# Kernel optimization log

Hardware: AMD Instinct MI355X
Metric: run time of the kernel (lower is better)

Reference implementation:

```python
import jax, jax.numpy as jnp
import numpy as np

N_HEADS = 16
N_KV_HEADS = 4
N_EMBED = 2048
HEAD_DIM = 128
SECTIONS = [16, 24, 24, 16, 24, 24]


def _process_rotary(c):
    # c: [3, B, T, HEAD_DIM] -> [B, 1, T, HEAD_DIM]
    splits = np.cumsum(SECTIONS)[:-1]
    secs = jnp.split(c, splits, axis=-1)
    out = jnp.concatenate([s[i % 3] for i, s in enumerate(secs)], axis=-1)
    return out[:, None]  # add head axis


def _rotate_half(x):
    x1, x2 = jnp.split(x, 2, axis=-1)
    return jnp.concatenate([-x2, x1], axis=-1)


def setup_inputs() -> dict:
    key = jax.random.key(0)
    ks = jax.random.split(key, 12)
    B, T = 1, 2048
    s = 0.02
    return {
        "x": jax.random.normal(ks[0], (B, T, N_EMBED), jnp.float32),
        "cos": jax.random.uniform(ks[1], (3, B, T, HEAD_DIM), jnp.float32),
        "sin": jax.random.uniform(ks[2], (3, B, T, HEAD_DIM), jnp.float32),
        "Wq": jax.random.normal(ks[3], (N_EMBED, N_EMBED), jnp.float32) * s,
        "bq": jax.random.normal(ks[4], (N_EMBED,), jnp.float32) * s,
        "Wk": jax.random.normal(ks[5], (N_EMBED, N_KV_HEADS * HEAD_DIM), jnp.float32) * s,
        "bk": jax.random.normal(ks[6], (N_KV_HEADS * HEAD_DIM,), jnp.float32) * s,
        "Wv": jax.random.normal(ks[7], (N_EMBED, N_KV_HEADS * HEAD_DIM), jnp.float32) * s,
        "bv": jax.random.normal(ks[8], (N_KV_HEADS * HEAD_DIM,), jnp.float32) * s,
        "Wo": jax.random.normal(ks[9], (N_EMBED, N_EMBED), jnp.float32) * s,
    }


def reference(x, cos, sin, Wq, bq, Wk, bk, Wv, bv, Wo):
    B, T, C = x.shape
    H, Hkv, D = N_HEADS, N_KV_HEADS, HEAD_DIM
    q = (x @ Wq + bq).reshape(B, T, H, D).transpose(0, 2, 1, 3)    # [B,H,T,D]
    k = (x @ Wk + bk).reshape(B, T, Hkv, D).transpose(0, 2, 1, 3)  # [B,Hkv,T,D]
    v = (x @ Wv + bv).reshape(B, T, Hkv, D).transpose(0, 2, 1, 3)
    # multi-section rope (cos/sin are 4-dim -> custom path)
    c = _process_rotary(cos)
    s = _process_rotary(sin)
    q = q * c + _rotate_half(q) * s
    k = k * c + _rotate_half(k) * s
    present_k, present_v = k, v
    # GQA expansion (repeat_interleave over head axis)
    r = H // Hkv
    k = jnp.repeat(k, r, axis=1)
    v = jnp.repeat(v, r, axis=1)
    # causal SDPA
    scores = jnp.einsum("bhqd,bhkd->bhqk", q, k) / jnp.sqrt(jnp.float32(D))
    causal = jnp.tril(jnp.ones((T, T), dtype=bool))
    scores = jnp.where(causal, scores, jnp.finfo(scores.dtype).min)
    attn = jax.nn.softmax(scores, axis=-1)
    y = jnp.einsum("bhqk,bhkd->bhqd", attn, v)
    y = y.transpose(0, 2, 1, 3).reshape(B, T, C)
    y = y @ Wo
    return (y, present_k, present_v)
```

## Files before the change

kernel.cpp:

```cpp
#include <hip/hip_runtime.h>

typedef unsigned short u16;
typedef unsigned int u32;
typedef __attribute__((ext_vector_type(4))) float f32x4;
typedef __attribute__((ext_vector_type(8))) __bf16 bf16x8;
typedef __attribute__((ext_vector_type(4))) u16 u16x4;
typedef __attribute__((ext_vector_type(2))) u32 u32x2;


__device__ __forceinline__ u16 f2bf(float f) {
  union { float f; unsigned u; } v; v.f = f;
  unsigned r = v.u + 0x7fffu + ((v.u >> 16) & 1u);
  return (u16)(r >> 16);
}

__device__ __forceinline__ u32 pack_bf2(float a, float b) {
  union { float f; unsigned u; } x, y;
  x.f = a; y.f = b;
#if __has_builtin(__builtin_amdgcn_perm)
  return __builtin_amdgcn_perm(y.u + 0x8000u, x.u + 0x8000u, 0x07060302u);
#else
  return (u32)((x.u + 0x8000u) >> 16) | ((y.u + 0x8000u) & 0xffff0000u);
#endif
}

__device__ __forceinline__ void stage16(const void* g, void* l) {
#if __has_builtin(__builtin_amdgcn_global_load_lds)
  __builtin_amdgcn_global_load_lds((const __attribute__((address_space(1))) void*)g,
                                   (__attribute__((address_space(3))) void*)l, 16, 0, 0);
#else
  *(f32x4*)l = *(const f32x4*)g;
#endif
}

__device__ __forceinline__ f32x4 mfma16(bf16x8 a, bf16x8 b, f32x4 c) {
  return __builtin_amdgcn_mfma_f32_16x16x32_bf16(a, b, c, 0, 0, 0);
}

__device__ __forceinline__ float fexp2(float x) {
#if __has_builtin(__builtin_amdgcn_exp2f)
  return __builtin_amdgcn_exp2f(x);
#else
  return exp2f(x);
#endif
}

__device__ __forceinline__ int rope_ch(int d) {
  int dd = (d < 64) ? d : d - 64;
  return (dd < 16) ? 0 : (dd < 40 ? 1 : 2);
}


__global__ void yuna_convert_prep(const float* __restrict__ in, u16* __restrict__ out,
                                  const float* __restrict__ cosp, const float* __restrict__ sinp,
                                  float* __restrict__ csel, float* __restrict__ ssel) {
  int b = blockIdx.x;
  if (b < 4096) {
    int i = b * 256 + threadIdx.x;
    f32x4 v = ((const f32x4*)in)[i];
    u16x4 o;
    o.x = f2bf(v.x); o.y = f2bf(v.y); o.z = f2bf(v.z); o.w = f2bf(v.w);
    ((u16x4*)out)[i] = o;
  } else {
    int i = (b - 4096) * 256 + threadIdx.x;
    int i4 = i * 4;
    int t = i4 >> 7, d = i4 & 127;
    f32x4 c, s;
#pragma unroll
    for (int j = 0; j < 4; ++j) {
      int ch = rope_ch(d + j);
      c[j] = cosp[(size_t)ch * 262144 + (size_t)t * 128 + d + j];
      s[j] = sinp[(size_t)ch * 262144 + (size_t)t * 128 + d + j];
    }
    ((f32x4*)csel)[i] = c;
    ((f32x4*)ssel)[i] = s;
  }
}

__global__ void yuna_prep_weights(const float* __restrict__ Wq, const float* __restrict__ Wk,
                                  const float* __restrict__ Wv, const float* __restrict__ Wo,
                                  u16* __restrict__ Wb, u16* __restrict__ Wob) {
  __shared__ float tile[64][65];
  const int mat = blockIdx.z;
  const float* W;
  u16* out;
  int N;
  if (mat == 0)      { W = Wq; out = Wb;                          N = 2048; }
  else if (mat == 1) { W = Wk; out = Wb + (size_t)2048 * 2048;    N = 512; }
  else if (mat == 2) { W = Wv; out = Wb + (size_t)2560 * 2048;    N = 512; }
  else               { W = Wo; out = Wob;                         N = 2048; }
  int k0 = blockIdx.x * 64, n0 = blockIdx.y * 64;
  if (n0 >= N) return;
  int tx = threadIdx.x & 63, ty = threadIdx.x >> 6;
#pragma unroll
  for (int j = 0; j < 64; j += 4)
    tile[ty + j][tx] = W[(size_t)(k0 + ty + j) * N + n0 + tx];
  __syncthreads();
#pragma unroll
  for (int j = 0; j < 64; j += 4)
    out[(size_t)(n0 + ty + j) * 2048 + k0 + tx] = f2bf(tile[tx][ty + j]);
}

__global__ __launch_bounds__(256, 3) void yuna_gemm_qkv(
    const u16* __restrict__ A, const u16* __restrict__ Bt,
    const float* __restrict__ bq, const float* __restrict__ bk, const float* __restrict__ bv,
    const float* __restrict__ csel, const float* __restrict__ ssel,
    u16* __restrict__ qb, u16* __restrict__ kb, u16* __restrict__ vtb,
    float* __restrict__ pk, float* __restrict__ pv) {
  const int K = 2048;
  __shared__ __align__(16) char smem[49152];
  const int tid = threadIdx.x;
  const int wave = tid >> 6, lane = tid & 63;
  const int lrow = lane & 15, lkg = lane >> 4;
  const int m0 = blockIdx.x * 64;
  const int by = blockIdx.y;
  const int n0 = by * 128;
  const int sw = lrow & 7;

  const int srow = tid >> 3;
  const int ssc = (tid & 7) ^ ((tid >> 3) & 7);
  const size_t abase = (size_t)(m0 + srow) * K + ssc * 8;
  const size_t bbase = (size_t)(n0 + srow) * K + ssc * 8;

  const f32x4 fzero = {0.f, 0.f, 0.f, 0.f};
  f32x4 acc[4][2];
#pragma unroll
  for (int mi = 0; mi < 4; ++mi) { acc[mi][0] = fzero; acc[mi][1] = fzero; }

#pragma unroll
  for (int it = 0; it < 2; ++it)
    stage16(A + abase + (size_t)it * 32 * K, smem + (tid + it * 256) * 16);
#pragma unroll
  for (int it = 0; it < 4; ++it)
    stage16(Bt + bbase + (size_t)it * 32 * K, smem + 16384 + (tid + it * 256) * 16);

  for (int k0 = 0, ki = 0; k0 < K; k0 += 64, ++ki) {
    const int cur = ki & 1;
    const char* Asb = smem + cur * 8192;
    const char* Bsb = smem + 16384 + cur * 16384;
    if (k0 + 64 < K) {
      char* Asn = smem + (cur ^ 1) * 8192;
      char* Bsn = smem + 16384 + (cur ^ 1) * 16384;
#pragma unroll
      for (int it = 0; it < 2; ++it)
        stage16(A + abase + (size_t)it * 32 * K + k0 + 64, Asn + (tid + it * 256) * 16);
#pragma unroll
      for (int it = 0; it < 4; ++it)
        stage16(Bt + bbase + (size_t)it * 32 * K + k0 + 64, Bsn + (tid + it * 256) * 16);
      asm volatile("s_waitcnt vmcnt(6)\n\ts_barrier" ::: "memory");
    } else {
      asm volatile("s_waitcnt vmcnt(0)\n\ts_barrier" ::: "memory");
    }
#pragma unroll
    for (int kk = 0; kk < 2; ++kk) {
      const int cof = ((kk * 4 + lkg) ^ sw) << 4;
      bf16x8 af[4], bfr[2];
#pragma unroll
      for (int mi = 0; mi < 4; ++mi)
        af[mi] = *(const bf16x8*)(Asb + (mi * 16 + lrow) * 128 + cof);
#pragma unroll
      for (int ni = 0; ni < 2; ++ni)
        bfr[ni] = *(const bf16x8*)(Bsb + (wave * 16 + ni * 64 + lrow) * 128 + cof);
#pragma unroll
      for (int mi = 0; mi < 4; ++mi)
#pragma unroll
        for (int ni = 0; ni < 2; ++ni)
          acc[mi][ni] = mfma16(af[mi], bfr[ni], acc[mi][ni]);
    }
    asm volatile("s_barrier" ::: "memory");
  }

  if (by >= 20) {
    const int kvh = by - 20;
#pragma unroll
    for (int mi = 0; mi < 4; ++mi)
#pragma unroll
      for (int ni = 0; ni < 2; ++ni) {
        int d = wave * 16 + ni * 64 + lrow;
        float bb = bv[kvh * 128 + d];
        int mb = mi * 16 + lkg * 4;
        float v0 = acc[mi][ni][0] + bb, v1 = acc[mi][ni][1] + bb;
        float v2 = acc[mi][ni][2] + bb, v3 = acc[mi][ni][3] + bb;
        size_t pb = ((size_t)(kvh * 2048 + m0 + mb)) * 128 + d;
        pv[pb] = v0; pv[pb + 128] = v1; pv[pb + 256] = v2; pv[pb + 384] = v3;
        u16x4 w;
        w.x = f2bf(v0); w.y = f2bf(v1); w.z = f2bf(v2); w.w = f2bf(v3);
        *(u16x4*)(vtb + ((size_t)(kvh * 128 + d)) * 2048 + m0 + mb) = w;
      }
  } else {
    const float QSCALE = 1.4426950408889634f * 0.08838834764831845f;
    const bool isQ = (by < 16);
    const int h = isQ ? by : (by - 16);
    const float* bias = isQ ? bq : bk;
    const int dlo = wave * 16 + lrow;
    const float blo = bias[h * 128 + dlo];
    const float bhi = bias[h * 128 + dlo + 64];
#pragma unroll
    for (int mi = 0; mi < 4; ++mi) {
      const int tb = m0 + mi * 16 + lkg * 4;
#pragma unroll
      for (int r = 0; r < 4; ++r) {
        const int t = tb + r;
        float a = acc[mi][0][r] + blo;
        float b = acc[mi][1][r] + bhi;
        size_t cb = (size_t)t * 128 + dlo;
        float cl = csel[cb], sl = ssel[cb];
        float ch = csel[cb + 64], sh = ssel[cb + 64];
        float lo = a * cl - b * sl;
        float hi = b * ch + a * sh;
        size_t o = (((size_t)(h * 2048 + t)) << 7) + dlo;
        if (isQ) {
          qb[o] = f2bf(lo * QSCALE);
          qb[o + 64] = f2bf(hi * QSCALE);
        } else {
          kb[o] = f2bf(lo);
          kb[o + 64] = f2bf(hi);
          pk[o] = lo; pk[o + 64] = hi;
        }
      }
    }
  }
}

__global__ __launch_bounds__(256, 3) void yuna_gemm_out(
    const u16* __restrict__ A, const u16* __restrict__ Bt, float* __restrict__ C) {
  const int K = 2048;
  __shared__ __align__(16) char smem[49152];
  const int tid = threadIdx.x;
  const int wave = tid >> 6, lane = tid & 63;
  const int lrow = lane & 15, lkg = lane >> 4;
  const int m0 = blockIdx.x * 64;
  const int n0 = blockIdx.y * 128;
  const int wc = wave * 32;
  const int sw = lrow & 7;

  const int srow = tid >> 3;
  const int ssc = (tid & 7) ^ ((tid >> 3) & 7);
  const size_t abase = (size_t)(m0 + srow) * K + ssc * 8;
  const size_t bbase = (size_t)(n0 + srow) * K + ssc * 8;

  const f32x4 fzero = {0.f, 0.f, 0.f, 0.f};
  f32x4 acc[4][2];
#pragma unroll
  for (int mi = 0; mi < 4; ++mi) { acc[mi][0] = fzero; acc[mi][1] = fzero; }

#pragma unroll
  for (int it = 0; it < 2; ++it)
    stage16(A + abase + (size_t)it * 32 * K, smem + (tid + it * 256) * 16);
#pragma unroll
  for (int it = 0; it < 4; ++it)
    stage16(Bt + bbase + (size_t)it * 32 * K, smem + 16384 + (tid + it * 256) * 16);

  for (int k0 = 0, ki = 0; k0 < K; k0 += 64, ++ki) {
    const int cur = ki & 1;
    const char* Asb = smem + cur * 8192;
    const char* Bsb = smem + 16384 + cur * 16384;
    if (k0 + 64 < K) {
      char* Asn = smem + (cur ^ 1) * 8192;
      char* Bsn = smem + 16384 + (cur ^ 1) * 16384;
#pragma unroll
      for (int it = 0; it < 2; ++it)
        stage16(A + abase + (size_t)it * 32 * K + k0 + 64, Asn + (tid + it * 256) * 16);
#pragma unroll
      for (int it = 0; it < 4; ++it)
        stage16(Bt + bbase + (size_t)it * 32 * K + k0 + 64, Bsn + (tid + it * 256) * 16);
      asm volatile("s_waitcnt vmcnt(6)\n\ts_barrier" ::: "memory");
    } else {
      asm volatile("s_waitcnt vmcnt(0)\n\ts_barrier" ::: "memory");
    }
#pragma unroll
    for (int kk = 0; kk < 2; ++kk) {
      const int cof = ((kk * 4 + lkg) ^ sw) << 4;
      bf16x8 af[4], bfr[2];
#pragma unroll
      for (int mi = 0; mi < 4; ++mi)
        af[mi] = *(const bf16x8*)(Asb + (mi * 16 + lrow) * 128 + cof);
#pragma unroll
      for (int ni = 0; ni < 2; ++ni)
        bfr[ni] = *(const bf16x8*)(Bsb + (wc + ni * 16 + lrow) * 128 + cof);
#pragma unroll
      for (int mi = 0; mi < 4; ++mi)
#pragma unroll
        for (int ni = 0; ni < 2; ++ni)
          acc[mi][ni] = mfma16(af[mi], bfr[ni], acc[mi][ni]);
    }
    asm volatile("s_barrier" ::: "memory");
  }
#pragma unroll
  for (int mi = 0; mi < 4; ++mi)
#pragma unroll
    for (int ni = 0; ni < 2; ++ni) {
      int d = wc + ni * 16 + lrow;
      int mb = mi * 16 + lkg * 4;
#pragma unroll
      for (int r = 0; r < 4; ++r)
        C[(size_t)(m0 + mb + r) * 2048 + n0 + d] = acc[mi][ni][r];
    }
}

__global__ __launch_bounds__(256, 2) void yuna_flash_attn(
    const u16* __restrict__ Q,
    const u16* __restrict__ Kb,
    const u16* __restrict__ Vt,
    u16* __restrict__ Y) {
  __shared__ __align__(16) u16 Ks[2][64 * 128];
  __shared__ __align__(16) u16 Vs[2][128 * 64];
  __shared__ __align__(16) u16 Ps[64 * 64];
  const int h = blockIdx.x;
  const int yb = blockIdx.y;
  const int qb = (yb < 16) ? yb : 47 - yb;
  const int kvh = h >> 2;
  const int tid = threadIdx.x, wave = tid >> 6, lane = tid & 63;
  const int lrow = lane & 15, lkg = lane >> 4;
  const int m = wave * 16 + lrow;
  const int sw = lrow & 7;

  const int krow = tid >> 4;
  const int ksc = (tid & 15) ^ ((tid >> 4) & 7);
  const size_t kbase0 = ((size_t)(kvh * 2048 + krow) << 7) + ksc * 8;
  const int vrow = tid >> 3;
  const int vsc = (tid & 7) ^ ((tid >> 3) & 7);
  const size_t vbase0 = (size_t)(kvh * 128 + vrow) * 2048 + vsc * 8;

  bf16x8 qf[4];
#pragma unroll
  for (int kk = 0; kk < 4; ++kk)
    qf[kk] = *(const bf16x8*)(Q + (((size_t)h * 2048 + qb * 64 + m) << 7) + kk * 32 + lkg * 8);

  const f32x4 fzero = {0.f, 0.f, 0.f, 0.f};
  f32x4 o[8];
#pragma unroll
  for (int dt = 0; dt < 8; ++dt) o[dt] = fzero;
  float m_i = -1e30f, l_i = 0.f;

  const int nkb = qb + 1;

#pragma unroll
  for (int it = 0; it < 4; ++it)
    stage16(Kb + kbase0 + ((size_t)(it * 16) << 7), (char*)Ks[0] + (tid + it * 256) * 16);
#pragma unroll
  for (int it = 0; it < 4; ++it)
    stage16(Vt + vbase0 + (size_t)it * 32 * 2048, (char*)Vs[0] + (tid + it * 256) * 16);

  for (int kb = 0; kb < nkb; ++kb) {
    const int cur = kb & 1;
    const char* Ksb = (const char*)Ks[cur];
    const char* Vsb = (const char*)Vs[cur];
    if (kb + 1 < nkb) {
      char* Ksn = (char*)Ks[cur ^ 1];
      char* Vsn = (char*)Vs[cur ^ 1];
#pragma unroll
      for (int it = 0; it < 4; ++it)
        stage16(Kb + kbase0 + ((size_t)((kb + 1) * 64 + it * 16) << 7), Ksn + (tid + it * 256) * 16);
#pragma unroll
      for (int it = 0; it < 4; ++it)
        stage16(Vt + vbase0 + (size_t)it * 32 * 2048 + (kb + 1) * 64, Vsn + (tid + it * 256) * 16);
      asm volatile("s_waitcnt vmcnt(8)\n\ts_barrier" ::: "memory");
    } else {
      asm volatile("s_waitcnt vmcnt(0)\n\ts_barrier" ::: "memory");
    }

    f32x4 s[4];
#pragma unroll
    for (int nt = 0; nt < 4; ++nt) s[nt] = fzero;
#pragma unroll
    for (int kk = 0; kk < 4; ++kk) {
      const int cof = ((kk * 4 + lkg) ^ sw) << 4;
      bf16x8 kf[4];
#pragma unroll
      for (int nt = 0; nt < 4; ++nt)
        kf[nt] = *(const bf16x8*)(Ksb + (nt * 16 + lrow) * 256 + cof);
#pragma unroll
      for (int nt = 0; nt < 4; ++nt)
        s[nt] = mfma16(kf[nt], qf[kk], s[nt]);
    }
    if (kb == qb) {
#pragma unroll
      for (int nt = 0; nt < 4; ++nt)
#pragma unroll
        for (int r = 0; r < 4; ++r)
          if (nt * 16 + lkg * 4 + r > m) s[nt][r] = -1e30f;
    }

    float mx = -1e30f;
#pragma unroll
    for (int nt = 0; nt < 4; ++nt)
#pragma unroll
      for (int r = 0; r < 4; ++r) mx = fmaxf(mx, s[nt][r]);
    mx = fmaxf(mx, __shfl_xor(mx, 16));
    mx = fmaxf(mx, __shfl_xor(mx, 32));
    float mnew = fmaxf(m_i, mx);
    float alpha = fexp2(m_i - mnew);
    m_i = mnew;
    float ps = 0.f;
    const int hh = lkg & 1;
#pragma unroll
    for (int nt = 0; nt < 4; ++nt) {
      float p0 = fexp2(s[nt][0] - mnew);
      float p1 = fexp2(s[nt][1] - mnew);
      float p2 = fexp2(s[nt][2] - mnew);
      float p3 = fexp2(s[nt][3] - mnew);
      ps += (p0 + p1) + (p2 + p3);
      u32x2 pk2;
      pk2.x = pack_bf2(p0, p1);
      pk2.y = pack_bf2(p2, p3);
      int cc = 2 * nt + (lkg >> 1);
      *(u32x2*)((char*)Ps + m * 128 + ((cc ^ (m & 7)) << 4) + hh * 8) = pk2;
    }
    ps += __shfl_xor(ps, 16);
    ps += __shfl_xor(ps, 32);
    l_i = l_i * alpha + ps;
#pragma unroll
    for (int dt = 0; dt < 8; ++dt) o[dt] *= alpha;

#pragma unroll
    for (int kk = 0; kk < 2; ++kk) {
      const int cof = ((kk * 4 + lkg) ^ sw) << 4;
      bf16x8 pf = *(const bf16x8*)((char*)Ps + m * 128 + cof);
      bf16x8 vf[8];
#pragma unroll
      for (int dt = 0; dt < 8; ++dt)
        vf[dt] = *(const bf16x8*)(Vsb + (dt * 16 + lrow) * 128 + cof);
#pragma unroll
      for (int dt = 0; dt < 8; ++dt)
        o[dt] = mfma16(vf[dt], pf, o[dt]);
    }
    asm volatile("s_barrier" ::: "memory");
  }

  __syncthreads();
  {
    float inv = 1.f / l_i;
    const int hh = lkg & 1;
#pragma unroll
    for (int dt = 0; dt < 8; ++dt) {
      u32x2 w2;
      w2.x = pack_bf2(o[dt][0] * inv, o[dt][1] * inv);
      w2.y = pack_bf2(o[dt][2] * inv, o[dt][3] * inv);
      int cc = 2 * dt + (lkg >> 1);
      *(u32x2*)((char*)Ks[0] + m * 256 + ((cc ^ (m & 7)) << 4) + hh * 8) = w2;
    }
  }
  __syncthreads();
#pragma unroll
  for (int it = 0; it < 4; ++it) {
    int c = tid + it * 256;
    int row = c >> 4, cc = c & 15;
    f32x4 v = *(const f32x4*)((const char*)Ks[0] + row * 256 + ((cc ^ (row & 7)) << 4));
    *(f32x4*)(Y + (size_t)(qb * 64 + row) * 2048 + h * 128 + cc * 8) = v;
  }
}


extern "C" void kernel_launch(void* const* d_in, const int* in_sizes, int n_in,
                              void* d_out, int out_size, void* d_ws, size_t ws_size,
                              hipStream_t stream) {
  const float* x = (const float*)d_in[0];
  const float* cosp = (const float*)d_in[1];
  const float* sinp = (const float*)d_in[2];
  const float* Wq = (const float*)d_in[3];
  const float* bq = (const float*)d_in[4];
  const float* Wk = (const float*)d_in[5];
  const float* bk = (const float*)d_in[6];
  const float* Wv = (const float*)d_in[7];
  const float* bv = (const float*)d_in[8];
  const float* Wo = (const float*)d_in[9];
  float* out = (float*)d_out;
  float* out_k = out + 4194304;
  float* out_v = out + 5242880;

  char* ws = (char*)d_ws;
  u16* xb   = (u16*)(ws + 0);
  u16* Wb   = (u16*)(ws + 8388608);
  u16* Wob  = (u16*)(ws + 20971520);
  float* csel = (float*)(ws + 29360128);
  float* ssel = (float*)(ws + 30408704);
  u16* qbuf = (u16*)(ws + 54525952);
  u16* kbuf = (u16*)(ws + 62914560);
  u16* vtb  = (u16*)(ws + 65011712);
  u16* yat  = (u16*)(ws + 67108864);

  yuna_convert_prep<<<4352, 256, 0, stream>>>(x, xb, cosp, sinp, csel, ssel);
  yuna_prep_weights<<<dim3(32, 32, 4), 256, 0, stream>>>(Wq, Wk, Wv, Wo, Wb, Wob);
  yuna_gemm_qkv<<<dim3(32, 24), 256, 0, stream>>>(xb, Wb, bq, bk, bv, csel, ssel,
                                                  qbuf, kbuf, vtb, out_k, out_v);
  yuna_flash_attn<<<dim3(16, 32), 256, 0, stream>>>(qbuf, kbuf, vtb, yat);
  yuna_gemm_out<<<dim3(32, 16), 256, 0, stream>>>(yat, Wob, out);
}
```

Measured before the change: 227.0 us.

## Replace direct-to-LDS double buffering with register-staged single-buffer prefetch in GEMMs

Both projection GEMM kernels stop issuing async global-to-LDS copies into a double-buffered 48KB shared area. They now prefetch the next K tile into registers while computing on a single 24KB LDS buffer, then write the registers to LDS between barriers. This halves the LDS footprint, which may allow more resident blocks, at the cost of extra VGPRs, an extra barrier per iteration, and less overlap between loads and LDS writes.

```diff
diff --git a/kernel.cpp b/kernel.cpp
--- a/kernel.cpp
+++ b/kernel.cpp
@@ -108,7 +108,8 @@
     u16* __restrict__ qb, u16* __restrict__ kb, u16* __restrict__ vtb,
     float* __restrict__ pk, float* __restrict__ pv) {
   const int K = 2048;
-  __shared__ __align__(16) char smem[49152];
+  __shared__ __align__(16) char As[8192];
+  __shared__ __align__(16) char Bs[16384];
   const int tid = threadIdx.x;
   const int wave = tid >> 6, lane = tid & 63;
   const int lrow = lane & 15, lkg = lane >> 4;
@@ -127,29 +128,30 @@
 #pragma unroll
   for (int mi = 0; mi < 4; ++mi) { acc[mi][0] = fzero; acc[mi][1] = fzero; }
 
+  f32x4 areg[2], breg[4];
 #pragma unroll
   for (int it = 0; it < 2; ++it)
-    stage16(A + abase + (size_t)it * 32 * K, smem + (tid + it * 256) * 16);
+    areg[it] = *(const f32x4*)(A + abase + (size_t)it * 32 * K);
 #pragma unroll
   for (int it = 0; it < 4; ++it)
-    stage16(Bt + bbase + (size_t)it * 32 * K, smem + 16384 + (tid + it * 256) * 16);
-
-  for (int k0 = 0, ki = 0; k0 < K; k0 += 64, ++ki) {
-    const int cur = ki & 1;
-    const char* Asb = smem + cur * 8192;
-    const char* Bsb = smem + 16384 + cur * 16384;
-    if (k0 + 64 < K) {
-      char* Asn = smem + (cur ^ 1) * 8192;
-      char* Bsn = smem + 16384 + (cur ^ 1) * 16384;
+    breg[it] = *(const f32x4*)(Bt + bbase + (size_t)it * 32 * K);
+#pragma unroll
+  for (int it = 0; it < 2; ++it)
+    *(f32x4*)(As + (tid + it * 256) * 16) = areg[it];
+#pragma unroll
+  for (int it = 0; it < 4; ++it)
+    *(f32x4*)(Bs + (tid + it * 256) * 16) = breg[it];
+  __syncthreads();
+
+  for (int k0 = 0; k0 < K; k0 += 64) {
+    const bool more = (k0 + 64 < K);
+    if (more) {
 #pragma unroll
       for (int it = 0; it < 2; ++it)
-        stage16(A + abase + (size_t)it * 32 * K + k0 + 64, Asn + (tid + it * 256) * 16);
+        areg[it] = *(const f32x4*)(A + abase + (size_t)it * 32 * K + k0 + 64);
 #pragma unroll
       for (int it = 0; it < 4; ++it)
-        stage16(Bt + bbase + (size_t)it * 32 * K + k0 + 64, Bsn + (tid + it * 256) * 16);
-      asm volatile("s_waitcnt vmcnt(6)\n\ts_barrier" ::: "memory");
-    } else {
-      asm volatile("s_waitcnt vmcnt(0)\n\ts_barrier" ::: "memory");
+        breg[it] = *(const f32x4*)(Bt + bbase + (size_t)it * 32 * K + k0 + 64);
     }
 #pragma unroll
     for (int kk = 0; kk < 2; ++kk) {
@@ -157,17 +159,26 @@
       bf16x8 af[4], bfr[2];
 #pragma unroll
       for (int mi = 0; mi < 4; ++mi)
-        af[mi] = *(const bf16x8*)(Asb + (mi * 16 + lrow) * 128 + cof);
+        af[mi] = *(const bf16x8*)(As + (mi * 16 + lrow) * 128 + cof);
 #pragma unroll
       for (int ni = 0; ni < 2; ++ni)
-        bfr[ni] = *(const bf16x8*)(Bsb + (wave * 16 + ni * 64 + lrow) * 128 + cof);
+        bfr[ni] = *(const bf16x8*)(Bs + (wave * 16 + ni * 64 + lrow) * 128 + cof);
 #pragma unroll
       for (int mi = 0; mi < 4; ++mi)
 #pragma unroll
         for (int ni = 0; ni < 2; ++ni)
           acc[mi][ni] = mfma16(af[mi], bfr[ni], acc[mi][ni]);
     }
-    asm volatile("s_barrier" ::: "memory");
+    __syncthreads();
+    if (more) {
+#pragma unroll
+      for (int it = 0; it < 2; ++it)
+        *(f32x4*)(As + (tid + it * 256) * 16) = areg[it];
+#pragma unroll
+      for (int it = 0; it < 4; ++it)
+        *(f32x4*)(Bs + (tid + it * 256) * 16) = breg[it];
+      __syncthreads();
+    }
   }
 
   if (by >= 20) {
@@ -225,7 +236,8 @@
 __global__ __launch_bounds__(256, 3) void yuna_gemm_out(
     const u16* __restrict__ A, const u16* __restrict__ Bt, float* __restrict__ C) {
   const int K = 2048;
-  __shared__ __align__(16) char smem[49152];
+  __shared__ __align__(16) char As[8192];
+  __shared__ __align__(16) char Bs[16384];
   const int tid = threadIdx.x;
   const int wave = tid >> 6, lane = tid & 63;
   const int lrow = lane & 15, lkg = lane >> 4;
@@ -244,29 +256,30 @@
 #pragma unroll
   for (int mi = 0; mi < 4; ++mi) { acc[mi][0] = fzero; acc[mi][1] = fzero; }
 
+  f32x4 areg[2], breg[4];
 #pragma unroll
   for (int it = 0; it < 2; ++it)
-    stage16(A + abase + (size_t)it * 32 * K, smem + (tid + it * 256) * 16);
+    areg[it] = *(const f32x4*)(A + abase + (size_t)it * 32 * K);
 #pragma unroll
   for (int it = 0; it < 4; ++it)
-    stage16(Bt + bbase + (size_t)it * 32 * K, smem + 16384 + (tid + it * 256) * 16);
-
-  for (int k0 = 0, ki = 0; k0 < K; k0 += 64, ++ki) {
-    const int cur = ki & 1;
-    const char* Asb = smem + cur * 8192;
-    const char* Bsb = smem + 16384 + cur * 16384;
-    if (k0 + 64 < K) {
-      char* Asn = smem + (cur ^ 1) * 8192;
-      char* Bsn = smem + 16384 + (cur ^ 1) * 16384;
+    breg[it] = *(const f32x4*)(Bt + bbase + (size_t)it * 32 * K);
+#pragma unroll
+  for (int it = 0; it < 2; ++it)
+    *(f32x4*)(As + (tid + it * 256) * 16) = areg[it];
+#pragma unroll
+  for (int it = 0; it < 4; ++it)
+    *(f32x4*)(Bs + (tid + it * 256) * 16) = breg[it];
+  __syncthreads();
+
+  for (int k0 = 0; k0 < K; k0 += 64) {
+    const bool more = (k0 + 64 < K);
+    if (more) {
 #pragma unroll
       for (int it = 0; it < 2; ++it)
-        stage16(A + abase + (size_t)it * 32 * K + k0 + 64, Asn + (tid + it * 256) * 16);
+        areg[it] = *(const f32x4*)(A + abase + (size_t)it * 32 * K + k0 + 64);
 #pragma unroll
       for (int it = 0; it < 4; ++it)
-        stage16(Bt + bbase + (size_t)it * 32 * K + k0 + 64, Bsn + (tid + it * 256) * 16);
-      asm volatile("s_waitcnt vmcnt(6)\n\ts_barrier" ::: "memory");
-    } else {
-      asm volatile("s_waitcnt vmcnt(0)\n\ts_barrier" ::: "memory");
+        breg[it] = *(const f32x4*)(Bt + bbase + (size_t)it * 32 * K + k0 + 64);
     }
 #pragma unroll
     for (int kk = 0; kk < 2; ++kk) {
@@ -274,17 +287,26 @@
       bf16x8 af[4], bfr[2];
 #pragma unroll
       for (int mi = 0; mi < 4; ++mi)
-        af[mi] = *(const bf16x8*)(Asb + (mi * 16 + lrow) * 128 + cof);
+        af[mi] = *(const bf16x8*)(As + (mi * 16 + lrow) * 128 + cof);
 #pragma unroll
       for (int ni = 0; ni < 2; ++ni)
-        bfr[ni] = *(const bf16x8*)(Bsb + (wc + ni * 16 + lrow) * 128 + cof);
+        bfr[ni] = *(const bf16x8*)(Bs + (wc + ni * 16 + lrow) * 128 + cof);
 #pragma unroll
       for (int mi = 0; mi < 4; ++mi)
 #pragma unroll
         for (int ni = 0; ni < 2; ++ni)
           acc[mi][ni] = mfma16(af[mi], bfr[ni], acc[mi][ni]);
     }
-    asm volatile("s_barrier" ::: "memory");
+    __syncthreads();
+    if (more) {
+#pragma unroll
+      for (int it = 0; it < 2; ++it)
+        *(f32x4*)(As + (tid + it * 256) * 16) = areg[it];
+#pragma unroll
+      for (int it = 0; it < 4; ++it)
+        *(f32x4*)(Bs + (tid + it * 256) * 16) = breg[it];
+      __syncthreads();
+    }
   }
 #pragma unroll
   for (int mi = 0; mi < 4; ++mi)
```

New measurement: 235.9 us. 1.04x slower.

## Widen QKV and output GEMM tiles to 64x256 per block

Applied to the files above, without the earlier changes.

Both GEMM kernels now compute a 64x256 output tile per block instead of 64x128, doubling the B-tile in shared memory and giving each wave a 4x4 MFMA accumulator grid. The aim is more reuse of the A tile per load and fewer blocks. The QKV epilogue is remapped so each wave pair handles one head, and the RoPE pairing and bias indexing change to match. In exchange, shared memory and register use rise, occupancy drops to 2 blocks per CU, and the grids shrink to 384 and 256 blocks, which may underfill the 256 CUs.

```diff
diff --git a/kernel.cpp b/kernel.cpp
--- a/kernel.cpp
+++ b/kernel.cpp
@@ -101,20 +101,20 @@
     out[(size_t)(n0 + ty + j) * 2048 + k0 + tx] = f2bf(tile[tx][ty + j]);
 }
 
-__global__ __launch_bounds__(256, 3) void yuna_gemm_qkv(
+__global__ __launch_bounds__(256, 2) void yuna_gemm_qkv(
     const u16* __restrict__ A, const u16* __restrict__ Bt,
     const float* __restrict__ bq, const float* __restrict__ bk, const float* __restrict__ bv,
     const float* __restrict__ csel, const float* __restrict__ ssel,
     u16* __restrict__ qb, u16* __restrict__ kb, u16* __restrict__ vtb,
     float* __restrict__ pk, float* __restrict__ pv) {
   const int K = 2048;
-  __shared__ __align__(16) char smem[49152];
+  __shared__ __align__(16) char smem[81920];
   const int tid = threadIdx.x;
   const int wave = tid >> 6, lane = tid & 63;
   const int lrow = lane & 15, lkg = lane >> 4;
   const int m0 = blockIdx.x * 64;
   const int by = blockIdx.y;
-  const int n0 = by * 128;
+  const int n0 = by * 256;
   const int sw = lrow & 7;
 
   const int srow = tid >> 3;
@@ -122,61 +122,67 @@
   const size_t abase = (size_t)(m0 + srow) * K + ssc * 8;
   const size_t bbase = (size_t)(n0 + srow) * K + ssc * 8;
 
+  const int rbase = (wave >> 1) * 128 + (wave & 1) * 32 + lrow;
+
   const f32x4 fzero = {0.f, 0.f, 0.f, 0.f};
-  f32x4 acc[4][2];
-#pragma unroll
-  for (int mi = 0; mi < 4; ++mi) { acc[mi][0] = fzero; acc[mi][1] = fzero; }
+  f32x4 acc[4][4];
+#pragma unroll
+  for (int mi = 0; mi < 4; ++mi)
+#pragma unroll
+    for (int ni = 0; ni < 4; ++ni) acc[mi][ni] = fzero;
 
 #pragma unroll
   for (int it = 0; it < 2; ++it)
     stage16(A + abase + (size_t)it * 32 * K, smem + (tid + it * 256) * 16);
 #pragma unroll
-  for (int it = 0; it < 4; ++it)
+  for (int it = 0; it < 8; ++it)
     stage16(Bt + bbase + (size_t)it * 32 * K, smem + 16384 + (tid + it * 256) * 16);
 
   for (int k0 = 0, ki = 0; k0 < K; k0 += 64, ++ki) {
     const int cur = ki & 1;
     const char* Asb = smem + cur * 8192;
-    const char* Bsb = smem + 16384 + cur * 16384;
+    const char* Bsb = smem + 16384 + cur * 32768;
     if (k0 + 64 < K) {
       char* Asn = smem + (cur ^ 1) * 8192;
-      char* Bsn = smem + 16384 + (cur ^ 1) * 16384;
+      char* Bsn = smem + 16384 + (cur ^ 1) * 32768;
 #pragma unroll
       for (int it = 0; it < 2; ++it)
         stage16(A + abase + (size_t)it * 32 * K + k0 + 64, Asn + (tid + it * 256) * 16);
 #pragma unroll
-      for (int it = 0; it < 4; ++it)
+      for (int it = 0; it < 8; ++it)
         stage16(Bt + bbase + (size_t)it * 32 * K + k0 + 64, Bsn + (tid + it * 256) * 16);
-      asm volatile("s_waitcnt vmcnt(6)\n\ts_barrier" ::: "memory");
+      asm volatile("s_waitcnt vmcnt(10)\n\ts_barrier" ::: "memory");
     } else {
       asm volatile("s_waitcnt vmcnt(0)\n\ts_barrier" ::: "memory");
     }
 #pragma unroll
     for (int kk = 0; kk < 2; ++kk) {
       const int cof = ((kk * 4 + lkg) ^ sw) << 4;
-      bf16x8 af[4], bfr[2];
+      bf16x8 af[4], bfr[4];
 #pragma unroll
       for (int mi = 0; mi < 4; ++mi)
         af[mi] = *(const bf16x8*)(Asb + (mi * 16 + lrow) * 128 + cof);
 #pragma unroll
-      for (int ni = 0; ni < 2; ++ni)
-        bfr[ni] = *(const bf16x8*)(Bsb + (wave * 16 + ni * 64 + lrow) * 128 + cof);
+      for (int ni = 0; ni < 4; ++ni)
+        bfr[ni] = *(const bf16x8*)(Bsb + (rbase + (ni & 1) * 16 + (ni >> 1) * 64) * 128 + cof);
 #pragma unroll
       for (int mi = 0; mi < 4; ++mi)
 #pragma unroll
-        for (int ni = 0; ni < 2; ++ni)
+        for (int ni = 0; ni < 4; ++ni)
           acc[mi][ni] = mfma16(af[mi], bfr[ni], acc[mi][ni]);
     }
     asm volatile("s_barrier" ::: "memory");
   }
 
-  if (by >= 20) {
-    const int kvh = by - 20;
+  const int dlo0 = (wave & 1) * 32 + lrow;
+  const int dlo1 = dlo0 + 16;
+  if (by >= 10) {
+    const int kvh = (by - 10) * 2 + (wave >> 1);
 #pragma unroll
     for (int mi = 0; mi < 4; ++mi)
 #pragma unroll
-      for (int ni = 0; ni < 2; ++ni) {
-        int d = wave * 16 + ni * 64 + lrow;
+      for (int ni = 0; ni < 4; ++ni) {
+        int d = (wave & 1) * 32 + (ni & 1) * 16 + (ni >> 1) * 64 + lrow;
         float bb = bv[kvh * 128 + d];
         int mb = mi * 16 + lkg * 4;
         float v0 = acc[mi][ni][0] + bb, v1 = acc[mi][ni][1] + bb;
@@ -189,49 +195,65 @@
       }
   } else {
     const float QSCALE = 1.4426950408889634f * 0.08838834764831845f;
-    const bool isQ = (by < 16);
-    const int h = isQ ? by : (by - 16);
+    const bool isQ = (by < 8);
+    const int h = (isQ ? by * 2 : (by - 8) * 2) + (wave >> 1);
     const float* bias = isQ ? bq : bk;
-    const int dlo = wave * 16 + lrow;
-    const float blo = bias[h * 128 + dlo];
-    const float bhi = bias[h * 128 + dlo + 64];
+    const float blo0 = bias[h * 128 + dlo0], bhi0 = bias[h * 128 + dlo0 + 64];
+    const float blo1 = bias[h * 128 + dlo1], bhi1 = bias[h * 128 + dlo1 + 64];
 #pragma unroll
     for (int mi = 0; mi < 4; ++mi) {
       const int tb = m0 + mi * 16 + lkg * 4;
 #pragma unroll
       for (int r = 0; r < 4; ++r) {
         const int t = tb + r;
-        float a = acc[mi][0][r] + blo;
-        float b = acc[mi][1][r] + bhi;
-        size_t cb = (size_t)t * 128 + dlo;
-        float cl = csel[cb], sl = ssel[cb];
-        float ch = csel[cb + 64], sh = ssel[cb + 64];
-        float lo = a * cl - b * sl;
-        float hi = b * ch + a * sh;
-        size_t o = (((size_t)(h * 2048 + t)) << 7) + dlo;
-        if (isQ) {
-          qb[o] = f2bf(lo * QSCALE);
-          qb[o + 64] = f2bf(hi * QSCALE);
-        } else {
-          kb[o] = f2bf(lo);
-          kb[o + 64] = f2bf(hi);
-          pk[o] = lo; pk[o + 64] = hi;
+        const size_t trow = (size_t)t * 128;
+        const size_t o = (((size_t)(h * 2048 + t)) << 7);
+        {
+          float a = acc[mi][0][r] + blo0;
+          float b = acc[mi][2][r] + bhi0;
+          float cl = csel[trow + dlo0], sl = ssel[trow + dlo0];
+          float ch = csel[trow + dlo0 + 64], sh = ssel[trow + dlo0 + 64];
+          float lo = a * cl - b * sl;
+          float hi = b * ch + a * sh;
+          if (isQ) {
+            qb[o + dlo0] = f2bf(lo * QSCALE);
+            qb[o + dlo0 + 64] = f2bf(hi * QSCALE);
+          } else {
+            kb[o + dlo0] = f2bf(lo);
+            kb[o + dlo0 + 64] = f2bf(hi);
+            pk[o + dlo0] = lo; pk[o + dlo0 + 64] = hi;
+          }
+        }
+        {
+          float a = acc[mi][1][r] + blo1;
+          float b = acc[mi][3][r] + bhi1;
+          float cl = csel[trow + dlo1], sl = ssel[trow + dlo1];
+          float ch = csel[trow + dlo1 + 64], sh = ssel[trow + dlo1 + 64];
+          float lo = a * cl - b * sl;
+          float hi = b * ch + a * sh;
+          if (isQ) {
+            qb[o + dlo1] = f2bf(lo * QSCALE);
+            qb[o + dlo1 + 64] = f2bf(hi * QSCALE);
+          } else {
+            kb[o + dlo1] = f2bf(lo);
+            kb[o + dlo1 + 64] = f2bf(hi);
+            pk[o + dlo1] = lo; pk[o + dlo1 + 64] = hi;
+          }
         }
       }
     }
   }
 }
 
-__global__ __launch_bounds__(256, 3) void yuna_gemm_out(
+__global__ __launch_bounds__(256, 2) void yuna_gemm_out(
     const u16* __restrict__ A, const u16* __restrict__ Bt, float* __restrict__ C) {
   const int K = 2048;
-  __shared__ __align__(16) char smem[49152];
+  __shared__ __align__(16) char smem[81920];
   const int tid = threadIdx.x;
   const int wave = tid >> 6, lane = tid & 63;
   const int lrow = lane & 15, lkg = lane >> 4;
   const int m0 = blockIdx.x * 64;
-  const int n0 = blockIdx.y * 128;
-  const int wc = wave * 32;
+  const int n0 = blockIdx.y * 256;
   const int sw = lrow & 7;
 
   const int srow = tid >> 3;
@@ -240,48 +262,50 @@
   const size_t bbase = (size_t)(n0 + srow) * K + ssc * 8;
 
   const f32x4 fzero = {0.f, 0.f, 0.f, 0.f};
-  f32x4 acc[4][2];
-#pragma unroll
-  for (int mi = 0; mi < 4; ++mi) { acc[mi][0] = fzero; acc[mi][1] = fzero; }
+  f32x4 acc[4][4];
+#pragma unroll
+  for (int mi = 0; mi < 4; ++mi)
+#pragma unroll
+    for (int ni = 0; ni < 4; ++ni) acc[mi][ni] = fzero;
 
 #pragma unroll
   for (int it = 0; it < 2; ++it)
     stage16(A + abase + (size_t)it * 32 * K, smem + (tid + it * 256) * 16);
 #pragma unroll
-  for (int it = 0; it < 4; ++it)
+  for (int it = 0; it < 8; ++it)
     stage16(Bt + bbase + (size_t)it * 32 * K, smem + 16384 + (tid + it * 256) * 16);
 
   for (int k0 = 0, ki = 0; k0 < K; k0 += 64, ++ki) {
     const int cur = ki & 1;
     const char* Asb = smem + cur * 8192;
-    const char* Bsb = smem + 16384 + cur * 16384;
+    const char* Bsb = smem + 16384 + cur * 32768;
     if (k0 + 64 < K) {
       char* Asn = smem + (cur ^ 1) * 8192;
-      char* Bsn = smem + 16384 + (cur ^ 1) * 16384;
+      char* Bsn = smem + 16384 + (cur ^ 1) * 32768;
 #pragma unroll
       for (int it = 0; it < 2; ++it)
         stage16(A + abase + (size_t)it * 32 * K + k0 + 64, Asn + (tid + it * 256) * 16);
 #pragma unroll
-      for (int it = 0; it < 4; ++it)
+      for (int it = 0; it < 8; ++it)
         stage16(Bt + bbase + (size_t)it * 32 * K + k0 + 64, Bsn + (tid + it * 256) * 16);
-      asm volatile("s_waitcnt vmcnt(6)\n\ts_barrier" ::: "memory");
+      asm volatile("s_waitcnt vmcnt(10)\n\ts_barrier" ::: "memory");
     } else {
       asm volatile("s_waitcnt vmcnt(0)\n\ts_barrier" ::: "memory");
     }
 #pragma unroll
     for (int kk = 0; kk < 2; ++kk) {
       const int cof = ((kk * 4 + lkg) ^ sw) << 4;
-      bf16x8 af[4], bfr[2];
+      bf16x8 af[4], bfr[4];
 #pragma unroll
       for (int mi = 0; mi < 4; ++mi)
         af[mi] = *(const bf16x8*)(Asb + (mi * 16 + lrow) * 128 + cof);
 #pragma unroll
-      for (int ni = 0; ni < 2; ++ni)
-        bfr[ni] = *(const bf16x8*)(Bsb + (wc + ni * 16 + lrow) * 128 + cof);
+      for (int ni = 0; ni < 4; ++ni)
+        bfr[ni] = *(const bf16x8*)(Bsb + (wave * 64 + ni * 16 + lrow) * 128 + cof);
 #pragma unroll
       for (int mi = 0; mi < 4; ++mi)
 #pragma unroll
-        for (int ni = 0; ni < 2; ++ni)
+        for (int ni = 0; ni < 4; ++ni)
           acc[mi][ni] = mfma16(af[mi], bfr[ni], acc[mi][ni]);
     }
     asm volatile("s_barrier" ::: "memory");
@@ -289,12 +313,12 @@
 #pragma unroll
   for (int mi = 0; mi < 4; ++mi)
 #pragma unroll
-    for (int ni = 0; ni < 2; ++ni) {
-      int d = wc + ni * 16 + lrow;
+    for (int ni = 0; ni < 4; ++ni) {
+      int d = n0 + wave * 64 + ni * 16 + lrow;
       int mb = mi * 16 + lkg * 4;
 #pragma unroll
       for (int r = 0; r < 4; ++r)
-        C[(size_t)(m0 + mb + r) * 2048 + n0 + d] = acc[mi][ni][r];
+        C[(size_t)(m0 + mb + r) * 2048 + d] = acc[mi][ni][r];
     }
 }
 
@@ -482,8 +506,8 @@
 
   yuna_convert_prep<<<4352, 256, 0, stream>>>(x, xb, cosp, sinp, csel, ssel);
   yuna_prep_weights<<<dim3(32, 32, 4), 256, 0, stream>>>(Wq, Wk, Wv, Wo, Wb, Wob);
-  yuna_gemm_qkv<<<dim3(32, 24), 256, 0, stream>>>(xb, Wb, bq, bk, bv, csel, ssel,
+  yuna_gemm_qkv<<<dim3(32, 12), 256, 0, stream>>>(xb, Wb, bq, bk, bv, csel, ssel,
                                                   qbuf, kbuf, vtb, out_k, out_v);
   yuna_flash_attn<<<dim3(16, 32), 256, 0, stream>>>(qbuf, kbuf, vtb, yat);
-  yuna_gemm_out<<<dim3(32, 16), 256, 0, stream>>>(yat, Wob, out);
-}
+  yuna_gemm_out<<<dim3(32, 8), 256, 0, stream>>>(yat, Wob, out);
+}
```

Result: slower. 238.6 us (+5.1%).
